# Kernel tuning notes

Hardware: AMD Instinct MI355X
Metric: run time of the kernel (lower is better)

## Reference

```python
import jax, jax.numpy as jnp
import numpy as np

EMBED_DIM = 1024
NUM_HEADS = 16
HEAD_DIM = EMBED_DIM // NUM_HEADS
LN_EPS = 1e-12
B, S = 2, 2048


def setup_inputs() -> dict:
    key = jax.random.key(0)
    ks = jax.random.split(key, 12)
    scale = 1.0 / np.sqrt(EMBED_DIM)
    d = EMBED_DIM
    return {
        "in_features": jax.random.normal(ks[0], (B, S, d), dtype=jnp.float32),
        "tgt_mask": jnp.ones((B, S), dtype=jnp.float32),
        "Wq": jax.random.normal(ks[1], (d, d), dtype=jnp.float32) * scale,
        "bq": jnp.zeros((d,), dtype=jnp.float32),
        "Wk": jax.random.normal(ks[2], (d, d), dtype=jnp.float32) * scale,
        "bk": jnp.zeros((d,), dtype=jnp.float32),
        "Wv": jax.random.normal(ks[3], (d, d), dtype=jnp.float32) * scale,
        "bv": jnp.zeros((d,), dtype=jnp.float32),
        "Wo": jax.random.normal(ks[4], (d, d), dtype=jnp.float32) * scale,
        "bo": jnp.zeros((d,), dtype=jnp.float32),
        "gamma": jnp.ones((d,), dtype=jnp.float32),
        "beta": jnp.zeros((d,), dtype=jnp.float32),
    }


def _split_heads(x):  # [B,S,D] -> [B,H,S,Dh]
    b, s, _ = x.shape
    return x.reshape(b, s, NUM_HEADS, HEAD_DIM).transpose(0, 2, 1, 3)


def reference(in_features, tgt_mask, Wq, bq, Wk, bk, Wv, bv, Wo, bo, gamma, beta):
    # Self-attention (tgt_features defaults to in_features). Dropout in eval mode (identity).
    q = _split_heads(in_features @ Wq.T + bq)
    k = _split_heads(in_features @ Wk.T + bk)
    v = _split_heads(in_features @ Wv.T + bv)
    # scores: [B,H,S,S]
    scores = jnp.einsum("bhqd,bhkd->bhqk", q, k) / jnp.sqrt(jnp.float32(HEAD_DIM))
    scores = scores + (1.0 - tgt_mask)[:, None, None, :] * (-100000.0)
    attn = jax.nn.softmax(scores, axis=-1)
    ctx = jnp.einsum("bhqk,bhkd->bhqd", attn, v)  # [B,H,S,Dh]
    ctx = ctx.transpose(0, 2, 1, 3).reshape(in_features.shape)  # merge heads
    out = ctx @ Wo.T + bo
    x = out + in_features
    mu = jnp.mean(x, axis=-1, keepdims=True)
    var = jnp.mean(jnp.square(x - mu), axis=-1, keepdims=True)
    return (x - mu) / jnp.sqrt(var + LN_EPS) * gamma + beta
```

## Files before the change

### kernel.cpp

```cpp
#include <hip/hip_runtime.h>
#include <hip/hip_bf16.h>

#define DM   1024
#define HEADS 16
#define DH    64
#define SEQ  2048
#define BATCH   2
#define LOG2E 1.44269504088896f

typedef __attribute__((ext_vector_type(8))) short short8;
typedef __attribute__((ext_vector_type(4))) short bf16x4;
typedef __attribute__((ext_vector_type(4))) float floatx4;

__device__ __forceinline__ short f2b(float f) {
    union { float f; unsigned u; } v; v.f = f;
    unsigned r = v.u + 0x7FFFu + ((v.u >> 16) & 1u);
    return (short)(r >> 16);
}

#if __has_builtin(__builtin_amdgcn_exp2f)
__device__ __forceinline__ float fexp2(float x) { return __builtin_amdgcn_exp2f(x); }
#else
__device__ __forceinline__ float fexp2(float x) { return exp2f(x); }
#endif

__device__ __forceinline__ void async_copy16(const short* gsrc, short* ldst) {
    __builtin_amdgcn_global_load_lds(
        (const __attribute__((address_space(1))) void*)gsrc,
        (__attribute__((address_space(3))) void*)ldst,
        16, 0, 0);
}

__global__ __launch_bounds__(256) void cvt_all(const float* __restrict__ x,
        const float* __restrict__ wq, const float* __restrict__ wk,
        const float* __restrict__ wv, const float* __restrict__ wo,
        const float* __restrict__ mask,
        short* __restrict__ xb, short* __restrict__ wqkv, short* __restrict__ wob,
        float* __restrict__ maddg)
{
    const int b = blockIdx.x;
    if (b >= 8192) {
        const int bb = b - 8192;
        const float* mrow = mask + (size_t)bb * SEQ;
        float* mg = maddg + (size_t)bb * SEQ;
#pragma unroll
        for (int i = 0; i < 8; ++i) {
            const int idx = threadIdx.x * 8 + i;
            mg[idx] = (1.f - mrow[idx]) * (-100000.f * LOG2E);
        }
        return;
    }
    const float* src; short* dst; int idx;
    if (b < 4096)      { src = x;  dst = xb;                idx = b; }
    else if (b < 5120) { src = wq; dst = wqkv;              idx = b - 4096; }
    else if (b < 6144) { src = wk; dst = wqkv + (1 << 20);  idx = b - 5120; }
    else if (b < 7168) { src = wv; dst = wqkv + (2 << 20);  idx = b - 6144; }
    else               { src = wo; dst = wob;               idx = b - 7168; }
    const int i = idx * 256 + threadIdx.x;
    floatx4 v = ((const floatx4*)src)[i];
    bf16x4 o;
    o.x = f2b(v.x); o.y = f2b(v.y); o.z = f2b(v.z); o.w = f2b(v.w);
    ((bf16x4*)dst)[i] = o;
}

__global__ __launch_bounds__(256) void gemm_qkv(const short* __restrict__ A,
        const short* __restrict__ B,
        const float* __restrict__ bq, const float* __restrict__ bk,
        const float* __restrict__ bv,
        short* __restrict__ qw, short* __restrict__ kw, short* __restrict__ vw)
{
    __shared__ short As[128 * 32];
    __shared__ short Bs[128 * 32];
    const int m0 = blockIdx.x * 128, n0 = blockIdx.y * 128;
    const int w = threadIdx.x >> 6, lane = threadIdx.x & 63;
    const int l16 = lane & 15, quad = lane >> 4;
    const int wm = w >> 1, wn = w & 1;
    const int lr = lane >> 2, lc = (lane & 3) * 8;

    floatx4 acc[4][4];
#pragma unroll
    for (int i = 0; i < 4; ++i)
#pragma unroll
        for (int j = 0; j < 4; ++j) acc[i][j] = (floatx4){0.f, 0.f, 0.f, 0.f};

    for (int kt = 0; kt < DM / 32; ++kt) {
        const int k0 = kt * 32;
        __syncthreads();
        async_copy16(A + (size_t)(m0 + w * 32 + lr) * DM + k0 + lc,      &As[w * 1024]);
        async_copy16(A + (size_t)(m0 + w * 32 + 16 + lr) * DM + k0 + lc, &As[w * 1024 + 512]);
        async_copy16(B + (size_t)(n0 + w * 32 + lr) * DM + k0 + lc,      &Bs[w * 1024]);
        async_copy16(B + (size_t)(n0 + w * 32 + 16 + lr) * DM + k0 + lc, &Bs[w * 1024 + 512]);
        __syncthreads();

        short8 af[4], bf[4];
#pragma unroll
        for (int i = 0; i < 4; ++i)
            af[i] = *(const short8*)&As[(wm * 64 + i * 16 + l16) * 32 + quad * 8];
#pragma unroll
        for (int j = 0; j < 4; ++j)
            bf[j] = *(const short8*)&Bs[(wn * 64 + j * 16 + l16) * 32 + quad * 8];
#pragma unroll
        for (int i = 0; i < 4; ++i)
#pragma unroll
            for (int j = 0; j < 4; ++j)
                acc[i][j] = __builtin_amdgcn_mfma_f32_16x16x32_bf16(af[i], bf[j], acc[i][j], 0, 0, 0);
    }

    const int m_base = m0 + wm * 64 + quad * 4;
#pragma unroll
    for (int j = 0; j < 4; ++j) {
        const int nb = n0 + wn * 64 + j * 16;
        const int t = nb >> 10;
        const int nn = (nb & 1023) + l16;
        const int h = nn >> 6, dh = nn & 63;
        const float* bias = (t == 0) ? bq : (t == 1) ? bk : bv;
        short* dst = (t == 0) ? qw : (t == 1) ? kw : vw;
        const float mulf = (t == 0) ? (0.125f * LOG2E) : 1.0f;
        const float bvv = bias[nn];
#pragma unroll
        for (int i = 0; i < 4; ++i)
#pragma unroll
            for (int r = 0; r < 4; ++r) {
                const int m = m_base + i * 16 + r;
                const int b = m >> 11, s = m & (SEQ - 1);
                dst[(((size_t)(b * HEADS + h)) * SEQ + s) * DH + dh] =
                    f2b((acc[i][j][r] + bvv) * mulf);
            }
    }
}

__global__ __launch_bounds__(256) void transpose_v(const short* __restrict__ v,
                                                   short* __restrict__ vt)
{
    __shared__ short tl[64][72];
    const int st = blockIdx.x;
    const int bh = blockIdx.y;
    const int t = threadIdx.x;
    const int row = t >> 2, off = (t & 3) * 16;
    const short* vp = v + ((size_t)bh * SEQ + st * 64 + row) * DH + off;
    *(short8*)&tl[row][off]     = *(const short8*)vp;
    *(short8*)&tl[row][off + 8] = *(const short8*)(vp + 8);
    __syncthreads();
    short8 o0, o1;
#pragma unroll
    for (int j = 0; j < 8; ++j) { o0[j] = tl[off + j][row]; o1[j] = tl[off + 8 + j][row]; }
    short* op = vt + ((size_t)bh * DH + row) * SEQ + st * 64 + off;
    *(short8*)op = o0;
    *(short8*)(op + 8) = o1;
}

__global__ __launch_bounds__(256) void attn_kernel(const short* __restrict__ q,
        const short* __restrict__ k, const short* __restrict__ vt,
        const float* __restrict__ maddg, short* __restrict__ ctx)
{
    const int id    = blockIdx.x;
    const int qtile = id >> 5;
    const int bh    = id & 31;
    const int bidx  = bh >> 4;
    const int wave = threadIdx.x >> 6, lane = threadIdx.x & 63;
    const int l16 = lane & 15, quad = lane >> 4;
    const int lx = l16 & 7;

    __shared__ short k_lds[64 * 64];
    __shared__ short v_lds[64 * 64];
    __shared__ short p_lds[4][16 * 64];
    __shared__ short Ct[64 * 72];

    const short* kbase0 = k  + (size_t)bh * SEQ * DH;
    const short* vbase0 = vt + (size_t)bh * DH * SEQ;
    const float* mrow   = maddg + (size_t)bidx * SEQ;

    const int qrow = qtile * 64 + wave * 16 + l16;
    const short* qbase = q + ((size_t)bh * SEQ + qrow) * DH;
    short8 b_q[2];
#pragma unroll
    for (int ks = 0; ks < 2; ++ks)
        b_q[ks] = *(const short8*)(qbase + ks * 32 + quad * 8);

    floatx4 o[4];
    floatx4 l_acc = (floatx4){0.f, 0.f, 0.f, 0.f};
#pragma unroll
    for (int d = 0; d < 4; ++d) o[d] = (floatx4){0.f, 0.f, 0.f, 0.f};

    short8 ones;
#pragma unroll
    for (int j = 0; j < 8; ++j) ones[j] = (short)0x3F80;

    int srw[2], gg[2];
#pragma unroll
    for (int i = 0; i < 2; ++i) {
        const int slot = i * 256 + wave * 64 + lane;
        srw[i] = slot >> 3;
        gg[i]  = (slot & 7) ^ (srw[i] & 7);
    }

    for (int kt = 0; kt < SEQ / 64; ++kt) {
        __syncthreads();
        {
            const short* kbase = kbase0 + (size_t)(kt * 64) * DH;
            const short* vbase = vbase0 + kt * 64;
#pragma unroll
            for (int i = 0; i < 2; ++i) {
                async_copy16(kbase + srw[i] * DH + gg[i] * 8,
                             &k_lds[(i * 256 + wave * 64) * 8]);
                async_copy16(vbase + (size_t)srw[i] * SEQ + gg[i] * 8,
                             &v_lds[(i * 256 + wave * 64) * 8]);
            }
        }
        floatx4 md[4];
#pragma unroll
        for (int nt = 0; nt < 4; ++nt)
            md[nt] = *(const floatx4*)&mrow[kt * 64 + nt * 16 + quad * 4];
        __syncthreads();

#pragma unroll
        for (int nt = 0; nt < 4; ++nt) {
            floatx4 acc = md[nt];
#pragma unroll
            for (int ks = 0; ks < 2; ++ks) {
                short8 a = *(const short8*)
                    &k_lds[(nt * 16 + l16) * 64 + (((ks * 4 + quad) ^ lx) * 8)];
                acc = __builtin_amdgcn_mfma_f32_16x16x32_bf16(a, b_q[ks], acc, 0, 0, 0);
            }
            const float p0 = fexp2(fminf(acc[0], 40.f));
            const float p1 = fexp2(fminf(acc[1], 40.f));
            const float p2 = fexp2(fminf(acc[2], 40.f));
            const float p3 = fexp2(fminf(acc[3], 40.f));
            union { __hip_bfloat162 h[2]; bf16x4 v; } u;
            u.h[0] = __float22bfloat162_rn(make_float2(p0, p1));
            u.h[1] = __float22bfloat162_rn(make_float2(p2, p3));
            *(bf16x4*)&p_lds[wave][l16 * 64 +
                (((nt * 2 + (quad >> 1)) ^ lx) * 8) + (quad & 1) * 4] = u.v;
        }

#pragma unroll
        for (int ks2 = 0; ks2 < 2; ++ks2) {
            short8 pf = *(const short8*)
                &p_lds[wave][l16 * 64 + (((ks2 * 4 + quad) ^ lx) * 8)];
#pragma unroll
            for (int d = 0; d < 4; ++d) {
                short8 vf = *(const short8*)
                    &v_lds[(d * 16 + l16) * 64 + (((ks2 * 4 + quad) ^ lx) * 8)];
                o[d] = __builtin_amdgcn_mfma_f32_16x16x32_bf16(pf, vf, o[d], 0, 0, 0);
            }
            l_acc = __builtin_amdgcn_mfma_f32_16x16x32_bf16(pf, ones, l_acc, 0, 0, 0);
        }
    }

    const int h = bh & 15, bb = bh >> 4;
    float rl[4];
#pragma unroll
    for (int r = 0; r < 4; ++r) rl[r] = 1.f / l_acc[r];
    __syncthreads();
#pragma unroll
    for (int d = 0; d < 4; ++d)
#pragma unroll
        for (int r = 0; r < 4; ++r)
            Ct[(wave * 16 + quad * 4 + r) * 72 + d * 16 + l16] = f2b(o[d][r] * rl[r]);
    __syncthreads();
    {
        const int row = threadIdx.x >> 2, ch = threadIdx.x & 3;
        short8 v0 = *(const short8*)&Ct[row * 72 + ch * 16];
        short8 v1 = *(const short8*)&Ct[row * 72 + ch * 16 + 8];
        short* gp = ctx + ((size_t)(bb * SEQ + qtile * 64 + row)) * DM + h * 64 + ch * 16;
        *(short8*)gp = v0;
        *(short8*)(gp + 8) = v1;
    }
}

__global__ __launch_bounds__(256) void gemm_o(const short* __restrict__ A,
        const short* __restrict__ B, const float* __restrict__ bo,
        const float* __restrict__ xin, float* __restrict__ out)
{
    __shared__ short As[128 * 32];
    __shared__ short Bs[64 * 32];
    const int m0 = blockIdx.x * 128, n0 = blockIdx.y * 64;
    const int w = threadIdx.x >> 6, lane = threadIdx.x & 63;
    const int l16 = lane & 15, quad = lane >> 4;
    const int wm = w >> 1, wn = w & 1;

    floatx4 acc[4][2];
#pragma unroll
    for (int i = 0; i < 4; ++i)
#pragma unroll
        for (int j = 0; j < 2; ++j) acc[i][j] = (floatx4){0.f, 0.f, 0.f, 0.f};

    const int c0 = w * 64 + lane;

    for (int kt = 0; kt < DM / 32; ++kt) {
        const int k0 = kt * 32;
        __syncthreads();
        {
            const int ra0 = c0 >> 2,          ca0 = (c0 & 3) * 8;
            const int ra1 = (256 + c0) >> 2,  ca1 = (c0 & 3) * 8;
            async_copy16(A + (size_t)(m0 + ra0) * DM + k0 + ca0, &As[(w * 64) * 8]);
            async_copy16(A + (size_t)(m0 + ra1) * DM + k0 + ca1, &As[(256 + w * 64) * 8]);
            const int rb = c0 >> 2, cb = (c0 & 3) * 8;
            async_copy16(B + (size_t)(n0 + rb) * DM + k0 + cb,   &Bs[(w * 64) * 8]);
        }
        __syncthreads();

        short8 af[4], bf[2];
#pragma unroll
        for (int i = 0; i < 4; ++i)
            af[i] = *(const short8*)&As[(wm * 64 + i * 16 + l16) * 32 + quad * 8];
#pragma unroll
        for (int j = 0; j < 2; ++j)
            bf[j] = *(const short8*)&Bs[(wn * 32 + j * 16 + l16) * 32 + quad * 8];
#pragma unroll
        for (int i = 0; i < 4; ++i)
#pragma unroll
            for (int j = 0; j < 2; ++j)
                acc[i][j] = __builtin_amdgcn_mfma_f32_16x16x32_bf16(af[i], bf[j], acc[i][j], 0, 0, 0);
    }

    const int m_base = m0 + wm * 64 + quad * 4;
#pragma unroll
    for (int j = 0; j < 2; ++j) {
        const int n = n0 + wn * 32 + j * 16 + l16;
        const float bvv = bo[n];
#pragma unroll
        for (int i = 0; i < 4; ++i)
#pragma unroll
            for (int r = 0; r < 4; ++r) {
                const int m = m_base + i * 16 + r;
                const size_t idx = (size_t)m * DM + n;
                out[idx] = acc[i][j][r] + bvv + xin[idx];
            }
    }
}

__global__ __launch_bounds__(256) void ln_kernel(float* __restrict__ y,
        const float* __restrict__ gamma, const float* __restrict__ beta)
{
    const int row = blockIdx.x;
    const int t = threadIdx.x;
    const int wave = t >> 6, lane = t & 63;
    const floatx4 v = ((const floatx4*)(y + (size_t)row * DM))[t];
    float s  = v.x + v.y + v.z + v.w;
    float q2 = v.x * v.x + v.y * v.y + v.z * v.z + v.w * v.w;
#pragma unroll
    for (int off = 1; off < 64; off <<= 1) {
        s  += __shfl_xor(s, off);
        q2 += __shfl_xor(q2, off);
    }
    __shared__ float rs[4], rq[4];
    if (lane == 0) { rs[wave] = s; rq[wave] = q2; }
    __syncthreads();
    const float S  = rs[0] + rs[1] + rs[2] + rs[3];
    const float Q2 = rq[0] + rq[1] + rq[2] + rq[3];
    const float mu = S * (1.f / DM);
    float var = Q2 * (1.f / DM) - mu * mu;
    var = fmaxf(var, 0.f);
    const float rstd = rsqrtf(var + 1e-12f);
    const floatx4 g = ((const floatx4*)gamma)[t];
    const floatx4 bt = ((const floatx4*)beta)[t];
    floatx4 o;
    o.x = (v.x - mu) * rstd * g.x + bt.x;
    o.y = (v.y - mu) * rstd * g.y + bt.y;
    o.z = (v.z - mu) * rstd * g.z + bt.z;
    o.w = (v.w - mu) * rstd * g.w + bt.w;
    ((floatx4*)(y + (size_t)row * DM))[t] = o;
}

extern "C" void kernel_launch(void* const* d_in, const int* in_sizes, int n_in,
                              void* d_out, int out_size, void* d_ws, size_t ws_size,
                              hipStream_t stream) {
    const float* x     = (const float*)d_in[0];
    const float* mask  = (const float*)d_in[1];
    const float* Wq    = (const float*)d_in[2];
    const float* bq    = (const float*)d_in[3];
    const float* Wk    = (const float*)d_in[4];
    const float* bk    = (const float*)d_in[5];
    const float* Wv    = (const float*)d_in[6];
    const float* bv    = (const float*)d_in[7];
    const float* Wo    = (const float*)d_in[8];
    const float* bo    = (const float*)d_in[9];
    const float* gamma = (const float*)d_in[10];
    const float* beta  = (const float*)d_in[11];
    float* out = (float*)d_out;

    const size_t NTOK = (size_t)BATCH * SEQ * DM;
    const size_t WSZ  = (size_t)DM * DM;
    short* xb   = (short*)d_ws;
    short* wqkv = xb + NTOK;
    short* wob  = wqkv + 3 * WSZ;
    short* qw   = wob + WSZ;
    short* kw   = qw + NTOK;
    short* vw   = kw + NTOK;
    short* vtw  = vw + NTOK;
    short* ctxw = vw;
    float* maddg = (float*)(vtw + NTOK);

    dim3 blk(256);
    cvt_all<<<dim3(8194), blk, 0, stream>>>(x, Wq, Wk, Wv, Wo, mask, xb, wqkv, wob, maddg);
    gemm_qkv<<<dim3(32, 24), blk, 0, stream>>>(xb, wqkv, bq, bk, bv, qw, kw, vw);
    transpose_v<<<dim3(SEQ / 64, BATCH * HEADS), blk, 0, stream>>>(vw, vtw);
    attn_kernel<<<dim3(32 * 32), blk, 0, stream>>>(qw, kw, vtw, maddg, ctxw);
    gemm_o<<<dim3(32, 16), blk, 0, stream>>>(ctxw, wob, bo, x, out);
    ln_kernel<<<BATCH * SEQ, blk, 0, stream>>>(out, gamma, beta);
}
```

Measured before the change: 222.5 us.

## Switch attention kernel to 32x32x16 MFMA with 2x2 wave tiling

Reorganizes the attention inner loop so the four waves form a 2x2 grid over (query, key/head-dim) and use 32x32x16 bf16 MFMA instead of 16x16x32. The probability tile is shared across waves through LDS, and the row sums are computed with scalar adds and combined through a small LDS buffer, replacing the extra MFMA against a ones vector. The aim is fewer MFMA issues and fewer LDS fragment reads per FLOP. In exchange it adds an extra block-wide barrier per key tile and cross-wave dependence on the P tile.

```diff
diff --git a/kernel.cpp b/kernel.cpp
--- a/kernel.cpp
+++ b/kernel.cpp
@@ -11,6 +11,7 @@
 typedef __attribute__((ext_vector_type(8))) short short8;
 typedef __attribute__((ext_vector_type(4))) short bf16x4;
 typedef __attribute__((ext_vector_type(4))) float floatx4;
+typedef __attribute__((ext_vector_type(16))) float floatx16;
 
 __device__ __forceinline__ short f2b(float f) {
     union { float f; unsigned u; } v; v.f = f;
@@ -158,33 +159,30 @@
     const int bh    = id & 31;
     const int bidx  = bh >> 4;
     const int wave = threadIdx.x >> 6, lane = threadIdx.x & 63;
-    const int l16 = lane & 15, quad = lane >> 4;
-    const int lx = l16 & 7;
+    const int l32 = lane & 31, half = lane >> 5;
+    const int kw = wave & 1, qw = wave >> 1;
 
     __shared__ short k_lds[64 * 64];
     __shared__ short v_lds[64 * 64];
-    __shared__ short p_lds[4][16 * 64];
+    __shared__ short p_lds[64 * 64];
+    __shared__ float l_lds[4 * 64];
     __shared__ short Ct[64 * 72];
 
     const short* kbase0 = k  + (size_t)bh * SEQ * DH;
     const short* vbase0 = vt + (size_t)bh * DH * SEQ;
     const float* mrow   = maddg + (size_t)bidx * SEQ;
 
-    const int qrow = qtile * 64 + wave * 16 + l16;
+    const int qrow = qtile * 64 + qw * 32 + l32;
     const short* qbase = q + ((size_t)bh * SEQ + qrow) * DH;
-    short8 b_q[2];
-#pragma unroll
-    for (int ks = 0; ks < 2; ++ks)
-        b_q[ks] = *(const short8*)(qbase + ks * 32 + quad * 8);
-
-    floatx4 o[4];
-    floatx4 l_acc = (floatx4){0.f, 0.f, 0.f, 0.f};
-#pragma unroll
-    for (int d = 0; d < 4; ++d) o[d] = (floatx4){0.f, 0.f, 0.f, 0.f};
-
-    short8 ones;
-#pragma unroll
-    for (int j = 0; j < 8; ++j) ones[j] = (short)0x3F80;
+    short8 b_q[4];
+#pragma unroll
+    for (int kk = 0; kk < 4; ++kk)
+        b_q[kk] = *(const short8*)(qbase + kk * 16 + half * 8);
+
+    floatx16 oacc;
+#pragma unroll
+    for (int r = 0; r < 16; ++r) oacc[r] = 0.f;
+    float l_run = 0.f;
 
     int srw[2], gg[2];
 #pragma unroll
@@ -193,6 +191,8 @@
         srw[i] = slot >> 3;
         gg[i]  = (slot & 7) ^ (srw[i] & 7);
     }
+
+    const int prow = qw * 32 + l32;
 
     for (int kt = 0; kt < SEQ / 64; ++kt) {
         __syncthreads();
@@ -209,54 +209,72 @@
         }
         floatx4 md[4];
 #pragma unroll
-        for (int nt = 0; nt < 4; ++nt)
-            md[nt] = *(const floatx4*)&mrow[kt * 64 + nt * 16 + quad * 4];
-        __syncthreads();
-
-#pragma unroll
-        for (int nt = 0; nt < 4; ++nt) {
-            floatx4 acc = md[nt];
-#pragma unroll
-            for (int ks = 0; ks < 2; ++ks) {
-                short8 a = *(const short8*)
-                    &k_lds[(nt * 16 + l16) * 64 + (((ks * 4 + quad) ^ lx) * 8)];
-                acc = __builtin_amdgcn_mfma_f32_16x16x32_bf16(a, b_q[ks], acc, 0, 0, 0);
+        for (int g = 0; g < 4; ++g)
+            md[g] = *(const floatx4*)&mrow[kt * 64 + kw * 32 + 8 * g + 4 * half];
+        __syncthreads();
+
+        floatx16 s;
+#pragma unroll
+        for (int g = 0; g < 4; ++g)
+#pragma unroll
+            for (int r = 0; r < 4; ++r) s[g * 4 + r] = md[g][r];
+        {
+            const int krow = kw * 32 + l32;
+            const int ksw = krow & 7;
+#pragma unroll
+            for (int kk = 0; kk < 4; ++kk) {
+                const int c = kk * 2 + half;
+                short8 a = *(const short8*)&k_lds[krow * 64 + ((c ^ ksw) * 8)];
+                s = __builtin_amdgcn_mfma_f32_32x32x16_bf16(a, b_q[kk], s, 0, 0, 0);
             }
-            const float p0 = fexp2(fminf(acc[0], 40.f));
-            const float p1 = fexp2(fminf(acc[1], 40.f));
-            const float p2 = fexp2(fminf(acc[2], 40.f));
-            const float p3 = fexp2(fminf(acc[3], 40.f));
+        }
+
+        float lsum = 0.f;
+        const int psw = prow & 7;
+#pragma unroll
+        for (int g = 0; g < 4; ++g) {
+            const float p0 = fexp2(fminf(s[g * 4 + 0], 40.f));
+            const float p1 = fexp2(fminf(s[g * 4 + 1], 40.f));
+            const float p2 = fexp2(fminf(s[g * 4 + 2], 40.f));
+            const float p3 = fexp2(fminf(s[g * 4 + 3], 40.f));
+            lsum += (p0 + p1) + (p2 + p3);
             union { __hip_bfloat162 h[2]; bf16x4 v; } u;
             u.h[0] = __float22bfloat162_rn(make_float2(p0, p1));
             u.h[1] = __float22bfloat162_rn(make_float2(p2, p3));
-            *(bf16x4*)&p_lds[wave][l16 * 64 +
-                (((nt * 2 + (quad >> 1)) ^ lx) * 8) + (quad & 1) * 4] = u.v;
-        }
-
-#pragma unroll
-        for (int ks2 = 0; ks2 < 2; ++ks2) {
-            short8 pf = *(const short8*)
-                &p_lds[wave][l16 * 64 + (((ks2 * 4 + quad) ^ lx) * 8)];
-#pragma unroll
-            for (int d = 0; d < 4; ++d) {
-                short8 vf = *(const short8*)
-                    &v_lds[(d * 16 + l16) * 64 + (((ks2 * 4 + quad) ^ lx) * 8)];
-                o[d] = __builtin_amdgcn_mfma_f32_16x16x32_bf16(pf, vf, o[d], 0, 0, 0);
+            const int c = kw * 4 + g;
+            *(bf16x4*)&p_lds[prow * 64 + ((c ^ psw) * 8) + 4 * half] = u.v;
+        }
+        l_lds[(kw * 2 + half) * 64 + prow] = lsum;
+        __syncthreads();
+
+        l_run += l_lds[0 * 64 + prow] + l_lds[1 * 64 + prow]
+               + l_lds[2 * 64 + prow] + l_lds[3 * 64 + prow];
+
+        {
+            const int vrow = kw * 32 + l32;
+            const int vsw = vrow & 7;
+#pragma unroll
+            for (int kk = 0; kk < 4; ++kk) {
+                const int c = kk * 2 + half;
+                short8 av = *(const short8*)&v_lds[vrow * 64 + ((c ^ vsw) * 8)];
+                short8 bp = *(const short8*)&p_lds[prow * 64 + ((c ^ psw) * 8)];
+                oacc = __builtin_amdgcn_mfma_f32_32x32x16_bf16(av, bp, oacc, 0, 0, 0);
             }
-            l_acc = __builtin_amdgcn_mfma_f32_16x16x32_bf16(pf, ones, l_acc, 0, 0, 0);
         }
     }
 
     const int h = bh & 15, bb = bh >> 4;
-    float rl[4];
-#pragma unroll
-    for (int r = 0; r < 4; ++r) rl[r] = 1.f / l_acc[r];
-    __syncthreads();
-#pragma unroll
-    for (int d = 0; d < 4; ++d)
-#pragma unroll
-        for (int r = 0; r < 4; ++r)
-            Ct[(wave * 16 + quad * 4 + r) * 72 + d * 16 + l16] = f2b(o[d][r] * rl[r]);
+    const float rl = 1.f / l_run;
+#pragma unroll
+    for (int g = 0; g < 4; ++g) {
+        bf16x4 p;
+        p.x = f2b(oacc[g * 4 + 0] * rl);
+        p.y = f2b(oacc[g * 4 + 1] * rl);
+        p.z = f2b(oacc[g * 4 + 2] * rl);
+        p.w = f2b(oacc[g * 4 + 3] * rl);
+        const int dh = kw * 32 + 8 * g + 4 * half;
+        *(bf16x4*)&Ct[prow * 72 + dh] = p;
+    }
     __syncthreads();
     {
         const int row = threadIdx.x >> 2, ch = threadIdx.x & 3;
```

After: 221.2 us. Within noise of the previous version (-0.6%).
